# Performance work log

Measured on AMD Instinct MI355X. Metric: run time of the kernel, lower is better.

Reference implementation:

```python
import jax, jax.numpy as jnp
import numpy as np

EMB = 1024
HEADS = 16
HEAD_DIM = EMB // HEADS


def setup_inputs() -> dict:
    key = jax.random.key(0)
    ks = jax.random.split(key, 12)
    B, S = 4, 2048
    s = 1.0 / np.sqrt(EMB)
    inp = {
        "query": jax.random.normal(ks[0], (B, S, EMB), jnp.float32),
        "key": jax.random.normal(ks[1], (B, S, EMB), jnp.float32),
        "value": jax.random.normal(ks[2], (B, S, EMB), jnp.float32),
        "mask": jax.random.randint(ks[3], (B, 1, 1, S), 0, 2) > 0,
        "Wq": jax.random.normal(ks[4], (EMB, EMB), jnp.float32) * s,
        "bq": jax.random.normal(ks[5], (EMB,), jnp.float32) * s,
        "Wk": jax.random.normal(ks[6], (EMB, EMB), jnp.float32) * s,
        "bk": jax.random.normal(ks[7], (EMB,), jnp.float32) * s,
        "Wv": jax.random.normal(ks[8], (EMB, EMB), jnp.float32) * s,
        "bv": jax.random.normal(ks[9], (EMB,), jnp.float32) * s,
        "Wo": jax.random.normal(ks[10], (EMB, EMB), jnp.float32) * s,
        "bo": jax.random.normal(ks[11], (EMB,), jnp.float32) * s,
    }
    return inp


def _split(x):
    # (B, S, E) -> (B, H, S, D)
    B, S, _ = x.shape
    return x.reshape(B, S, HEADS, HEAD_DIM).transpose(0, 2, 1, 3)


def reference(query, key, value, mask, Wq, bq, Wk, bk, Wv, bv, Wo, bo):
    q = _split(query @ Wq + bq)
    k = _split(key @ Wk + bk)
    v = _split(value @ Wv + bv)
    scale = 1.0 / np.sqrt(HEAD_DIM).astype(np.float32)
    # (B, H, S, S) score matrix, explicitly materialized as in the original
    scores = jnp.einsum("bhqd,bhkd->bhqk", q, k) * scale
    scores = jnp.where(mask, scores, -jnp.inf)
    probs = jax.nn.softmax(scores, axis=-1)
    attn = jnp.einsum("bhqk,bhkd->bhqd", probs, v)
    B, _, S, _ = attn.shape
    out = attn.transpose(0, 2, 1, 3).reshape(B, S, EMB)
    return out @ Wo + bo
```

## Files before the change

kernel.cpp:

```cpp
#include <hip/hip_runtime.h>
#include <hip/hip_bf16.h>
#include <stdint.h>

#define EMB 1024
#define HEADS 16
#define HDIM 64
#define BATCH 4
#define SEQ 2048
#define MTOT (BATCH * SEQ)

typedef unsigned short u16;
typedef __attribute__((ext_vector_type(8))) short bf16x8;
typedef __attribute__((ext_vector_type(4))) float f32x4;

__device__ inline u16 f2bf(float f) {
    uint32_t u = __builtin_bit_cast(uint32_t, f);
    u += 0x7fffu + ((u >> 16) & 1u);
    return (u16)(u >> 16);
}

__device__ inline uint32_t pkbf(float a, float b) {
    __hip_bfloat162 h = __float22bfloat162_rn(make_float2(a, b));
    uint32_t r;
    __builtin_memcpy(&r, &h, 4);
    return r;
}

__device__ inline f32x4 mfma16(bf16x8 a, bf16x8 b, f32x4 c) {
    return __builtin_amdgcn_mfma_f32_16x16x32_bf16(a, b, c, 0, 0, 0);
}

#define GLDS16(gp, lp)                                                        \
    __builtin_amdgcn_global_load_lds(                                         \
        (const __attribute__((address_space(1))) void*)(gp),                  \
        (__attribute__((address_space(3))) void*)(lp), 16, 0, 0)

__global__ void mask_compact(const int* __restrict__ mask,
                             int* __restrict__ cnt, int* __restrict__ idx) {
    __shared__ int ps[256];
    const int b = blockIdx.x, tid = threadIdx.x;
    const int* mp = mask + (size_t)b * SEQ;
    int m[8], s = 0;
#pragma unroll
    for (int e = 0; e < 8; ++e) {
        m[e] = mp[tid * 8 + e] ? 1 : 0;
        s += m[e];
    }
    ps[tid] = s;
    __syncthreads();
    for (int off = 1; off < 256; off <<= 1) {
        int v = (tid >= off) ? ps[tid - off] : 0;
        __syncthreads();
        if (tid >= off) ps[tid] += v;
        __syncthreads();
    }
    const int total = ps[255];
    int r = ps[tid] - s;
#pragma unroll
    for (int e = 0; e < 8; ++e)
        if (m[e]) idx[b * SEQ + r++] = tid * 8 + e;
    if (tid == 0) cnt[b] = total;
}

__global__ void gather_cast(const float* __restrict__ src,
                            const int* __restrict__ idx,
                            const int* __restrict__ cnt,
                            u16* __restrict__ dst) {
    const int row = blockIdx.x;
    const int b = row >> 11, j = row & (SEQ - 1);
    const int cn = cnt[b];
    const int cp = (cn + 127) & ~127;
    if (j >= cp) return;
    const int c4 = threadIdx.x;
    float4 v = {0.f, 0.f, 0.f, 0.f};
    if (j < cn) {
        const int srow = idx[b * SEQ + j];
        v = ((const float4*)(src + (size_t)(b * SEQ + srow) * EMB))[c4];
    }
    ushort4 o;
    o.x = f2bf(v.x); o.y = f2bf(v.y); o.z = f2bf(v.z); o.w = f2bf(v.w);
    ((ushort4*)(dst + (size_t)row * EMB))[c4] = o;
}

__global__ void cast_f32_bf16(const float* __restrict__ src,
                              u16* __restrict__ dst, int n4) {
    int i = blockIdx.x * blockDim.x + threadIdx.x;
    if (i >= n4) return;
    float4 v = ((const float4*)src)[i];
    ushort4 o;
    o.x = f2bf(v.x); o.y = f2bf(v.y); o.z = f2bf(v.z); o.w = f2bf(v.w);
    ((ushort4*)dst)[i] = o;
}

__global__ void transpose_cast(const float* __restrict__ W,
                               u16* __restrict__ Wt) {
    __shared__ u16 T[64][65];
    const int kb = blockIdx.y * 64, nb = blockIdx.x * 64;
    const int tr = threadIdx.x >> 4;
    const int tc = (threadIdx.x & 15) * 4;
#pragma unroll
    for (int j = 0; j < 4; ++j) {
        int r = tr + j * 16;
        float4 v = *(const float4*)&W[(size_t)(kb + r) * EMB + nb + tc];
        T[tc + 0][r] = f2bf(v.x);
        T[tc + 1][r] = f2bf(v.y);
        T[tc + 2][r] = f2bf(v.z);
        T[tc + 3][r] = f2bf(v.w);
    }
    __syncthreads();
#pragma unroll
    for (int j = 0; j < 4; ++j) {
        int rr = tr + j * 16;
        ushort4 o;
        o.x = T[rr][tc]; o.y = T[rr][tc + 1];
        o.z = T[rr][tc + 2]; o.w = T[rr][tc + 3];
        *(ushort4*)&Wt[(size_t)(nb + rr) * EMB + kb + tc] = o;
    }
}

__global__ void transpose_v(const u16* __restrict__ Vp, u16* __restrict__ Vt,
                            const int* __restrict__ cnt) {
    __shared__ u16 T[64][65];
    const int h = blockIdx.x;
    const int b = blockIdx.y >> 5;
    const int s0 = (blockIdx.y & 31) * 64;
    const int cp = (cnt[b] + 127) & ~127;
    if (s0 >= cp) return;
    const int tr = threadIdx.x >> 3;
    const int tc = (threadIdx.x & 7) * 8;
#pragma unroll
    for (int j = 0; j < 2; ++j) {
        int sr = tr + j * 32;
        uint4 v = *(const uint4*)&Vp[(size_t)(b * SEQ + s0 + sr) * EMB +
                                     h * 64 + tc];
        const u16* p = (const u16*)&v;
#pragma unroll
        for (int e = 0; e < 8; ++e) T[tc + e][sr] = p[e];
    }
    __syncthreads();
#pragma unroll
    for (int j = 0; j < 2; ++j) {
        int d = tr + j * 32;
        u16 tmp[8];
#pragma unroll
        for (int e = 0; e < 8; ++e) tmp[e] = T[d][tc + e];
        const int base32 = s0 + (tc & 32);
        const int p0 = ((tc & 8) << 1) + ((tc & 16) >> 2);
        const size_t rowoff =
            ((size_t)(b * HEADS + h) * HDIM + d) * SEQ;
        *(uint2*)&Vt[rowoff + base32 + p0] = *(const uint2*)&tmp[0];
        *(uint2*)&Vt[rowoff + base32 + p0 + 8] = *(const uint2*)&tmp[4];
    }
}

template <bool OUT_BF16>
__global__ __launch_bounds__(256, 2) void gemm_bt(
    const u16* __restrict__ A, const u16* __restrict__ Bt,
    const float* __restrict__ bias, void* __restrict__ C,
    int M, int N, int K, float scale, const int* __restrict__ cnt) {
    __shared__ __align__(16) u16 As[2][128 * 32];
    __shared__ __align__(16) u16 Bs[2][128 * 32];
    const int m0 = blockIdx.y * 128, n0 = blockIdx.x * 128;
    if (cnt) {
        const int bb = m0 >> 11;
        const int cp = (cnt[bb] + 127) & ~127;
        if ((m0 & (SEQ - 1)) >= cp) return;
    }
    const int tid = threadIdx.x;
    const int w = tid >> 6, l = tid & 63;
    const int quad = l >> 4, l16 = l & 15;
    const int wm = (w >> 1) * 64, wn = (w & 1) * 64;

    auto stage = [&](int buf, int k0) {
#pragma unroll
        for (int i = 0; i < 2; ++i) {
            int c = (w * 2 + i) * 64 + l;
            int r = c >> 2;
            int sc = (c & 3) ^ ((r >> 1) & 3);
            GLDS16(A + (size_t)(m0 + r) * K + k0 + sc * 8, &As[buf][c * 8]);
            GLDS16(Bt + (size_t)(n0 + r) * K + k0 + sc * 8, &Bs[buf][c * 8]);
        }
    };

    f32x4 acc[4][4];
#pragma unroll
    for (int i = 0; i < 4; ++i)
#pragma unroll
        for (int j = 0; j < 4; ++j) acc[i][j] = (f32x4){0.f, 0.f, 0.f, 0.f};

    stage(0, 0);
    __syncthreads();

    int cur = 0;
    for (int k0 = 0; k0 < K; k0 += 32, cur ^= 1) {
        if (k0 + 32 < K) stage(cur ^ 1, k0 + 32);
        bf16x8 af[4], bfr[4];
#pragma unroll
        for (int mt = 0; mt < 4; ++mt) {
            int ra = wm + mt * 16 + l16;
            af[mt] = *(const bf16x8*)&As[cur][ra * 32 +
                                             ((quad ^ ((ra >> 1) & 3)) * 8)];
        }
#pragma unroll
        for (int nt = 0; nt < 4; ++nt) {
            int rb = wn + nt * 16 + l16;
            bfr[nt] = *(const bf16x8*)&Bs[cur][rb * 32 +
                                              ((quad ^ ((rb >> 1) & 3)) * 8)];
        }
#pragma unroll
        for (int mt = 0; mt < 4; ++mt)
#pragma unroll
            for (int nt = 0; nt < 4; ++nt)
                acc[mt][nt] = mfma16(af[mt], bfr[nt], acc[mt][nt]);
        __syncthreads();
    }

#pragma unroll
    for (int mt = 0; mt < 4; ++mt) {
#pragma unroll
        for (int nt = 0; nt < 4; ++nt) {
            int col = n0 + wn + nt * 16 + l16;
            float bv = bias[col];
#pragma unroll
            for (int r = 0; r < 4; ++r) {
                int row = m0 + wm + mt * 16 + quad * 4 + r;
                float v = (acc[mt][nt][r] + bv) * scale;
                if (OUT_BF16)
                    ((u16*)C)[(size_t)row * N + col] = f2bf(v);
                else
                    ((float*)C)[(size_t)row * N + col] = v;
            }
        }
    }
}

__global__ __launch_bounds__(256, 2) void attn_kernel(
    const u16* __restrict__ Qp, const u16* __restrict__ Kp,
    const u16* __restrict__ Vt, const int* __restrict__ cnt,
    u16* __restrict__ attnb) {
    __shared__ __align__(16) u16 Ks[2][128 * 64];
    __shared__ __align__(16) u16 Vts[2][64 * 128];

    const int tid = threadIdx.x;
    const int w = tid >> 6, l = tid & 63;
    const int quad = l >> 4, l16 = l & 15;

    const int nqb = SEQ / 128;
    const int qb = blockIdx.x % nqb;
    const int bh = blockIdx.x / nqb;
    const int b = bh / HEADS, h = bh % HEADS;
    const int q0 = qb * 128;
    const size_t head_off = (size_t)b * SEQ * EMB + (size_t)h * HDIM;
    const size_t vt_off = (size_t)bh * HDIM * SEQ;

    const int cn = cnt[b];
    const int ntile = ((cn + 127) & ~127) >> 7;

    auto stageKV = [&](int buf, int t) {
#pragma unroll
        for (int i = 0; i < 4; ++i) {
            int c = (w * 4 + i) * 64 + l;
            int r = c >> 3;
            int sc = (c & 7) ^ (r & 7);
            GLDS16(Kp + head_off + (size_t)(t * 128 + r) * EMB + sc * 8,
                   &Ks[buf][c * 8]);
        }
#pragma unroll
        for (int i = 0; i < 4; ++i) {
            int c = (w * 4 + i) * 64 + l;
            int r = c >> 4;
            int sc = (c & 15) ^ (r & 15);
            GLDS16(Vt + vt_off + (size_t)r * SEQ + t * 128 + sc * 8,
                   &Vts[buf][c * 8]);
        }
    };

    bf16x8 bq[2][2];
#pragma unroll
    for (int g = 0; g < 2; ++g) {
        const u16* qrow =
            Qp + head_off + (size_t)(q0 + w * 32 + g * 16 + l16) * EMB;
        bq[g][0] = *(const bf16x8*)(qrow + quad * 8);
        bq[g][1] = *(const bf16x8*)(qrow + 32 + quad * 8);
    }

    bf16x8 ones;
#pragma unroll
    for (int e = 0; e < 8; ++e) ones[e] = (short)0x3f80;

    stageKV(0, 0);
    __syncthreads();

    f32x4 OA[4], OB[4];
#pragma unroll
    for (int i = 0; i < 4; ++i) {
        OA[i] = (f32x4){0.f, 0.f, 0.f, 0.f};
        OB[i] = (f32x4){0.f, 0.f, 0.f, 0.f};
    }
    f32x4 LA = (f32x4){0.f, 0.f, 0.f, 0.f};
    f32x4 LB = (f32x4){0.f, 0.f, 0.f, 0.f};

    auto tilebody = [&](int t, bool last) {
        const int cur = t & 1;
        if (!last) stageKV(cur ^ 1, t + 1);
        const u16* ksb = Ks[cur];
        const u16* vsb = Vts[cur];

        uint32_t pk[2][8][2];
#pragma unroll
        for (int nt = 0; nt < 8; ++nt) {
            int rk = nt * 16 + l16;
            bf16x8 ka0 =
                *(const bf16x8*)&ksb[rk * 64 + ((quad ^ (rk & 7)) * 8)];
            bf16x8 ka1 =
                *(const bf16x8*)&ksb[rk * 64 + (((quad + 4) ^ (rk & 7)) * 8)];
#pragma unroll
            for (int g = 0; g < 2; ++g) {
                f32x4 s = (f32x4){0.f, 0.f, 0.f, 0.f};
                s = mfma16(ka0, bq[g][0], s);
                s = mfma16(ka1, bq[g][1], s);
                f32x4 p;
                if (last) {
                    const int kb = t * 128 + nt * 16 + quad * 4;
#pragma unroll
                    for (int r = 0; r < 4; ++r)
                        p[r] = __builtin_amdgcn_exp2f(
                            (kb + r < cn) ? s[r] : -30000.f);
                } else {
#pragma unroll
                    for (int r = 0; r < 4; ++r)
                        p[r] = __builtin_amdgcn_exp2f(s[r]);
                }
                pk[g][nt][0] = pkbf(p[0], p[1]);
                pk[g][nt][1] = pkbf(p[2], p[3]);
            }
        }

#pragma unroll
        for (int i = 0; i < 4; ++i) {
            union { bf16x8 v; uint32_t u[4]; } bpA, bpB;
            bpA.u[0] = pk[0][2 * i][0];
            bpA.u[1] = pk[0][2 * i][1];
            bpA.u[2] = pk[0][2 * i + 1][0];
            bpA.u[3] = pk[0][2 * i + 1][1];
            bpB.u[0] = pk[1][2 * i][0];
            bpB.u[1] = pk[1][2 * i][1];
            bpB.u[2] = pk[1][2 * i + 1][0];
            bpB.u[3] = pk[1][2 * i + 1][1];
            LA = mfma16(ones, bpA.v, LA);
            LB = mfma16(ones, bpB.v, LB);
#pragma unroll
            for (int dt = 0; dt < 4; ++dt) {
                int vd = dt * 16 + l16;
                bf16x8 ap = *(const bf16x8*)&vsb[vd * 128 +
                                                 (((4 * i + quad) ^ (vd & 15)) *
                                                  8)];
                OA[dt] = mfma16(ap, bpA.v, OA[dt]);
                OB[dt] = mfma16(ap, bpB.v, OB[dt]);
            }
        }

        __syncthreads();
    };

    for (int t = 0; t < ntile - 1; ++t) tilebody(t, false);
    tilebody(ntile - 1, true);

#pragma unroll
    for (int g = 0; g < 2; ++g) {
        float inv = 1.0f / (g == 0 ? LA[0] : LB[0]);
        const f32x4* O = (g == 0) ? OA : OB;
        const int orow = q0 + w * 32 + g * 16 + l16;
#pragma unroll
        for (int dt = 0; dt < 4; ++dt) {
            ushort4 o;
            o.x = f2bf(O[dt][0] * inv);
            o.y = f2bf(O[dt][1] * inv);
            o.z = f2bf(O[dt][2] * inv);
            o.w = f2bf(O[dt][3] * inv);
            *(uint2*)&attnb[head_off + (size_t)orow * EMB + dt * 16 +
                            quad * 4] = *(uint2*)&o;
        }
    }
}

extern "C" void kernel_launch(void* const* d_in, const int* in_sizes, int n_in,
                              void* d_out, int out_size, void* d_ws,
                              size_t ws_size, hipStream_t stream) {
    const float* query = (const float*)d_in[0];
    const float* key = (const float*)d_in[1];
    const float* value = (const float*)d_in[2];
    const int* mask = (const int*)d_in[3];
    const float* Wq = (const float*)d_in[4];
    const float* bq = (const float*)d_in[5];
    const float* Wk = (const float*)d_in[6];
    const float* bk = (const float*)d_in[7];
    const float* Wv = (const float*)d_in[8];
    const float* bv = (const float*)d_in[9];
    const float* Wo = (const float*)d_in[10];
    const float* bo = (const float*)d_in[11];

    char* ws = (char*)d_ws;
    const size_t MB = 1ull << 20;
    u16* xq = (u16*)(ws + 0 * MB);
    u16* xk = (u16*)(ws + 16 * MB);
    u16* xv = (u16*)(ws + 32 * MB);
    u16* Wqt = (u16*)(ws + 48 * MB);
    u16* Wkt = (u16*)(ws + 50 * MB);
    u16* Wvt = (u16*)(ws + 52 * MB);
    u16* Wot = (u16*)(ws + 54 * MB);
    u16* Qp = (u16*)(ws + 56 * MB);
    u16* Kp = (u16*)(ws + 72 * MB);
    u16* Vp = (u16*)(ws + 88 * MB);
    u16* attnb = (u16*)(ws + 104 * MB);
    u16* Vt = xq;

    int* cnt = (int*)d_out;
    int* idx = (int*)d_out + 64;

    mask_compact<<<BATCH, 256, 0, stream>>>(mask, cnt, idx);

    const int n4 = MTOT * EMB / 4;
    cast_f32_bf16<<<(n4 + 255) / 256, 256, 0, stream>>>(query, xq, n4);
    gather_cast<<<MTOT, 256, 0, stream>>>(key, idx, cnt, xk);
    gather_cast<<<MTOT, 256, 0, stream>>>(value, idx, cnt, xv);

    dim3 tgrid(EMB / 64, EMB / 64);
    transpose_cast<<<tgrid, 256, 0, stream>>>(Wq, Wqt);
    transpose_cast<<<tgrid, 256, 0, stream>>>(Wk, Wkt);
    transpose_cast<<<tgrid, 256, 0, stream>>>(Wv, Wvt);
    transpose_cast<<<tgrid, 256, 0, stream>>>(Wo, Wot);

    const float c2 = 0.125f * 1.44269504f;
    dim3 ggrid(EMB / 128, MTOT / 128);
    gemm_bt<true><<<ggrid, 256, 0, stream>>>(xq, Wqt, bq, Qp, MTOT, EMB, EMB,
                                             c2, nullptr);
    gemm_bt<true><<<ggrid, 256, 0, stream>>>(xk, Wkt, bk, Kp, MTOT, EMB, EMB,
                                             1.0f, cnt);
    gemm_bt<true><<<ggrid, 256, 0, stream>>>(xv, Wvt, bv, Vp, MTOT, EMB, EMB,
                                             1.0f, cnt);

    transpose_v<<<dim3(HEADS, MTOT / 64), 256, 0, stream>>>(Vp, Vt, cnt);

    attn_kernel<<<BATCH * HEADS * (SEQ / 128), 256, 0, stream>>>(Qp, Kp, Vt,
                                                                 cnt, attnb);

    gemm_bt<false><<<ggrid, 256, 0, stream>>>(attnb, Wot, bo, d_out, MTOT, EMB,
                                              EMB, 1.0f, nullptr);
}
```

Baseline: 342.0 us.

## Batch prep/transpose/QKV launches and fuse V transpose into GEMM epilogue

New measurement: 309.8 us. -9.4%, faster.

```diff
diff --git a/kernel.cpp b/kernel.cpp
--- a/kernel.cpp
+++ b/kernel.cpp
@@ -62,16 +62,28 @@
     if (tid == 0) cnt[b] = total;
 }
 
-__global__ void gather_cast(const float* __restrict__ src,
-                            const int* __restrict__ idx,
-                            const int* __restrict__ cnt,
-                            u16* __restrict__ dst) {
+__global__ void prep_cast(const float* __restrict__ query,
+                          const float* __restrict__ key,
+                          const float* __restrict__ value,
+                          const int* __restrict__ idx,
+                          const int* __restrict__ cnt, u16* __restrict__ xq,
+                          u16* __restrict__ xk, u16* __restrict__ xv) {
+    const int z = blockIdx.y;
     const int row = blockIdx.x;
+    const int c4 = threadIdx.x;
+    if (z == 0) {
+        float4 v = ((const float4*)(query + (size_t)row * EMB))[c4];
+        ushort4 o;
+        o.x = f2bf(v.x); o.y = f2bf(v.y); o.z = f2bf(v.z); o.w = f2bf(v.w);
+        ((ushort4*)(xq + (size_t)row * EMB))[c4] = o;
+        return;
+    }
     const int b = row >> 11, j = row & (SEQ - 1);
     const int cn = cnt[b];
     const int cp = (cn + 127) & ~127;
     if (j >= cp) return;
-    const int c4 = threadIdx.x;
+    const float* src = (z == 1) ? key : value;
+    u16* dst = (z == 1) ? xk : xv;
     float4 v = {0.f, 0.f, 0.f, 0.f};
     if (j < cn) {
         const int srow = idx[b * SEQ + j];
@@ -82,19 +94,16 @@
     ((ushort4*)(dst + (size_t)row * EMB))[c4] = o;
 }
 
-__global__ void cast_f32_bf16(const float* __restrict__ src,
-                              u16* __restrict__ dst, int n4) {
-    int i = blockIdx.x * blockDim.x + threadIdx.x;
-    if (i >= n4) return;
-    float4 v = ((const float4*)src)[i];
-    ushort4 o;
-    o.x = f2bf(v.x); o.y = f2bf(v.y); o.z = f2bf(v.z); o.w = f2bf(v.w);
-    ((ushort4*)dst)[i] = o;
-}
-
-__global__ void transpose_cast(const float* __restrict__ W,
-                               u16* __restrict__ Wt) {
+__global__ void transpose_cast4(const float* __restrict__ Wq,
+                                const float* __restrict__ Wk,
+                                const float* __restrict__ Wv,
+                                const float* __restrict__ Wo,
+                                u16* __restrict__ Wqt, u16* __restrict__ Wkt,
+                                u16* __restrict__ Wvt, u16* __restrict__ Wot) {
     __shared__ u16 T[64][65];
+    const int z = blockIdx.z;
+    const float* W = z == 0 ? Wq : (z == 1 ? Wk : (z == 2 ? Wv : Wo));
+    u16* Wt = z == 0 ? Wqt : (z == 1 ? Wkt : (z == 2 ? Wvt : Wot));
     const int kb = blockIdx.y * 64, nb = blockIdx.x * 64;
     const int tr = threadIdx.x >> 4;
     const int tc = (threadIdx.x & 15) * 4;
@@ -118,54 +127,121 @@
     }
 }
 
-__global__ void transpose_v(const u16* __restrict__ Vp, u16* __restrict__ Vt,
-                            const int* __restrict__ cnt) {
-    __shared__ u16 T[64][65];
-    const int h = blockIdx.x;
-    const int b = blockIdx.y >> 5;
-    const int s0 = (blockIdx.y & 31) * 64;
-    const int cp = (cnt[b] + 127) & ~127;
-    if (s0 >= cp) return;
-    const int tr = threadIdx.x >> 3;
-    const int tc = (threadIdx.x & 7) * 8;
-#pragma unroll
-    for (int j = 0; j < 2; ++j) {
-        int sr = tr + j * 32;
-        uint4 v = *(const uint4*)&Vp[(size_t)(b * SEQ + s0 + sr) * EMB +
-                                     h * 64 + tc];
-        const u16* p = (const u16*)&v;
-#pragma unroll
-        for (int e = 0; e < 8; ++e) T[tc + e][sr] = p[e];
-    }
+__global__ __launch_bounds__(256, 2) void gemm_qkv(
+    const u16* __restrict__ xq, const u16* __restrict__ xk,
+    const u16* __restrict__ xv, const u16* __restrict__ Wqt,
+    const u16* __restrict__ Wkt, const u16* __restrict__ Wvt,
+    const float* __restrict__ bq, const float* __restrict__ bk,
+    const float* __restrict__ bv, u16* __restrict__ Qp, u16* __restrict__ Kp,
+    u16* __restrict__ Vt, const int* __restrict__ cnt, float c2) {
+    __shared__ __align__(16) u16 As[2][128 * 32];
+    __shared__ __align__(16) u16 Bs[2][128 * 32];
+    const int z = blockIdx.z;
+    const int m0 = blockIdx.y * 128, n0 = blockIdx.x * 128;
+    const int bb = m0 >> 11;
+    if (z) {
+        const int cp = (cnt[bb] + 127) & ~127;
+        if ((m0 & (SEQ - 1)) >= cp) return;
+    }
+    const u16* A = z == 0 ? xq : (z == 1 ? xk : xv);
+    const u16* Bt = z == 0 ? Wqt : (z == 1 ? Wkt : Wvt);
+    const float* bias = z == 0 ? bq : (z == 1 ? bk : bv);
+
+    const int tid = threadIdx.x;
+    const int w = tid >> 6, l = tid & 63;
+    const int quad = l >> 4, l16 = l & 15;
+    const int wm = (w >> 1) * 64, wn = (w & 1) * 64;
+
+    auto stage = [&](int buf, int k0) {
+#pragma unroll
+        for (int i = 0; i < 2; ++i) {
+            int c = (w * 2 + i) * 64 + l;
+            int r = c >> 2;
+            int sc = (c & 3) ^ ((r >> 1) & 3);
+            GLDS16(A + (size_t)(m0 + r) * EMB + k0 + sc * 8, &As[buf][c * 8]);
+            GLDS16(Bt + (size_t)(n0 + r) * EMB + k0 + sc * 8, &Bs[buf][c * 8]);
+        }
+    };
+
+    f32x4 acc[4][4];
+#pragma unroll
+    for (int i = 0; i < 4; ++i)
+#pragma unroll
+        for (int j = 0; j < 4; ++j) acc[i][j] = (f32x4){0.f, 0.f, 0.f, 0.f};
+
+    stage(0, 0);
     __syncthreads();
-#pragma unroll
-    for (int j = 0; j < 2; ++j) {
-        int d = tr + j * 32;
-        u16 tmp[8];
-#pragma unroll
-        for (int e = 0; e < 8; ++e) tmp[e] = T[d][tc + e];
-        const int base32 = s0 + (tc & 32);
-        const int p0 = ((tc & 8) << 1) + ((tc & 16) >> 2);
-        const size_t rowoff =
-            ((size_t)(b * HEADS + h) * HDIM + d) * SEQ;
-        *(uint2*)&Vt[rowoff + base32 + p0] = *(const uint2*)&tmp[0];
-        *(uint2*)&Vt[rowoff + base32 + p0 + 8] = *(const uint2*)&tmp[4];
-    }
-}
-
-template <bool OUT_BF16>
-__global__ __launch_bounds__(256, 2) void gemm_bt(
+
+    int cur = 0;
+    for (int k0 = 0; k0 < EMB; k0 += 32, cur ^= 1) {
+        if (k0 + 32 < EMB) stage(cur ^ 1, k0 + 32);
+        bf16x8 af[4], bfr[4];
+#pragma unroll
+        for (int mt = 0; mt < 4; ++mt) {
+            int ra = wm + mt * 16 + l16;
+            af[mt] = *(const bf16x8*)&As[cur][ra * 32 +
+                                             ((quad ^ ((ra >> 1) & 3)) * 8)];
+        }
+#pragma unroll
+        for (int nt = 0; nt < 4; ++nt) {
+            int rb = wn + nt * 16 + l16;
+            bfr[nt] = *(const bf16x8*)&Bs[cur][rb * 32 +
+                                              ((quad ^ ((rb >> 1) & 3)) * 8)];
+        }
+#pragma unroll
+        for (int mt = 0; mt < 4; ++mt)
+#pragma unroll
+            for (int nt = 0; nt < 4; ++nt)
+                acc[mt][nt] = mfma16(af[mt], bfr[nt], acc[mt][nt]);
+        __syncthreads();
+    }
+
+    if (z < 2) {
+        u16* C = (z == 0) ? Qp : Kp;
+        const float scale = (z == 0) ? c2 : 1.0f;
+#pragma unroll
+        for (int mt = 0; mt < 4; ++mt) {
+#pragma unroll
+            for (int nt = 0; nt < 4; ++nt) {
+                int col = n0 + wn + nt * 16 + l16;
+                float bv_ = bias[col];
+#pragma unroll
+                for (int r = 0; r < 4; ++r) {
+                    int row = m0 + wm + mt * 16 + quad * 4 + r;
+                    C[(size_t)row * EMB + col] =
+                        f2bf((acc[mt][nt][r] + bv_) * scale);
+                }
+            }
+        }
+    } else {
+#pragma unroll
+        for (int mt = 0; mt < 4; ++mt) {
+            const int srow = (m0 & (SEQ - 1)) + wm + mt * 16 + quad * 4;
+            const int grp = srow & ~31;
+            const int perm = ((srow & 15) >> 2) * 8 + ((srow >> 4) & 1) * 4;
+#pragma unroll
+            for (int nt = 0; nt < 4; ++nt) {
+                int col = n0 + wn + nt * 16 + l16;
+                int h = col >> 6, d = col & 63;
+                float bv_ = bias[col];
+                ushort4 o;
+                o.x = f2bf(acc[mt][nt][0] + bv_);
+                o.y = f2bf(acc[mt][nt][1] + bv_);
+                o.z = f2bf(acc[mt][nt][2] + bv_);
+                o.w = f2bf(acc[mt][nt][3] + bv_);
+                *(uint2*)&Vt[((size_t)(bb * HEADS + h) * HDIM + d) * SEQ +
+                             grp + perm] = *(uint2*)&o;
+            }
+        }
+    }
+}
+
+__global__ __launch_bounds__(256, 2) void gemm_bt_f32(
     const u16* __restrict__ A, const u16* __restrict__ Bt,
-    const float* __restrict__ bias, void* __restrict__ C,
-    int M, int N, int K, float scale, const int* __restrict__ cnt) {
+    const float* __restrict__ bias, float* __restrict__ C, int K) {
     __shared__ __align__(16) u16 As[2][128 * 32];
     __shared__ __align__(16) u16 Bs[2][128 * 32];
     const int m0 = blockIdx.y * 128, n0 = blockIdx.x * 128;
-    if (cnt) {
-        const int bb = m0 >> 11;
-        const int cp = (cnt[bb] + 127) & ~127;
-        if ((m0 & (SEQ - 1)) >= cp) return;
-    }
     const int tid = threadIdx.x;
     const int w = tid >> 6, l = tid & 63;
     const int quad = l >> 4, l16 = l & 15;
@@ -220,15 +296,11 @@
 #pragma unroll
         for (int nt = 0; nt < 4; ++nt) {
             int col = n0 + wn + nt * 16 + l16;
-            float bv = bias[col];
+            float bv_ = bias[col];
 #pragma unroll
             for (int r = 0; r < 4; ++r) {
                 int row = m0 + wm + mt * 16 + quad * 4 + r;
-                float v = (acc[mt][nt][r] + bv) * scale;
-                if (OUT_BF16)
-                    ((u16*)C)[(size_t)row * N + col] = f2bf(v);
-                else
-                    ((float*)C)[(size_t)row * N + col] = v;
+                C[(size_t)row * EMB + col] = acc[mt][nt][r] + bv_;
             }
         }
     }
@@ -411,40 +483,27 @@
     u16* Wot = (u16*)(ws + 54 * MB);
     u16* Qp = (u16*)(ws + 56 * MB);
     u16* Kp = (u16*)(ws + 72 * MB);
-    u16* Vp = (u16*)(ws + 88 * MB);
+    u16* Vt = (u16*)(ws + 88 * MB);
     u16* attnb = (u16*)(ws + 104 * MB);
-    u16* Vt = xq;
 
     int* cnt = (int*)d_out;
     int* idx = (int*)d_out + 64;
 
     mask_compact<<<BATCH, 256, 0, stream>>>(mask, cnt, idx);
 
-    const int n4 = MTOT * EMB / 4;
-    cast_f32_bf16<<<(n4 + 255) / 256, 256, 0, stream>>>(query, xq, n4);
-    gather_cast<<<MTOT, 256, 0, stream>>>(key, idx, cnt, xk);
-    gather_cast<<<MTOT, 256, 0, stream>>>(value, idx, cnt, xv);
-
-    dim3 tgrid(EMB / 64, EMB / 64);
-    transpose_cast<<<tgrid, 256, 0, stream>>>(Wq, Wqt);
-    transpose_cast<<<tgrid, 256, 0, stream>>>(Wk, Wkt);
-    transpose_cast<<<tgrid, 256, 0, stream>>>(Wv, Wvt);
-    transpose_cast<<<tgrid, 256, 0, stream>>>(Wo, Wot);
+    prep_cast<<<dim3(MTOT, 3), 256, 0, stream>>>(query, key, value, idx, cnt,
+                                                 xq, xk, xv);
+
+    transpose_cast4<<<dim3(EMB / 64, EMB / 64, 4), 256, 0, stream>>>(
+        Wq, Wk, Wv, Wo, Wqt, Wkt, Wvt, Wot);
 
     const float c2 = 0.125f * 1.44269504f;
-    dim3 ggrid(EMB / 128, MTOT / 128);
-    gemm_bt<true><<<ggrid, 256, 0, stream>>>(xq, Wqt, bq, Qp, MTOT, EMB, EMB,
-                                             c2, nullptr);
-    gemm_bt<true><<<ggrid, 256, 0, stream>>>(xk, Wkt, bk, Kp, MTOT, EMB, EMB,
-                                             1.0f, cnt);
-    gemm_bt<true><<<ggrid, 256, 0, stream>>>(xv, Wvt, bv, Vp, MTOT, EMB, EMB,
-                                             1.0f, cnt);
-
-    transpose_v<<<dim3(HEADS, MTOT / 64), 256, 0, stream>>>(Vp, Vt, cnt);
+    gemm_qkv<<<dim3(EMB / 128, MTOT / 128, 3), 256, 0, stream>>>(
+        xq, xk, xv, Wqt, Wkt, Wvt, bq, bk, bv, Qp, Kp, Vt, cnt, c2);
 
     attn_kernel<<<BATCH * HEADS * (SEQ / 128), 256, 0, stream>>>(Qp, Kp, Vt,
                                                                  cnt, attnb);
 
-    gemm_bt<false><<<ggrid, 256, 0, stream>>>(attnb, Wot, bo, d_out, MTOT, EMB,
-                                              EMB, 1.0f, nullptr);
-}
+    gemm_bt_f32<<<dim3(EMB / 128, MTOT / 128), 256, 0, stream>>>(
+        attnb, Wot, bo, (float*)d_out, EMB);
+}
```
